# Performance work log

Hardware: AMD Instinct MI355X
Metric: run time of the kernel (lower is better)

Reference implementation:

```python
import jax, jax.numpy as jnp
import numpy as np

B, C, L, D = 8, 256, 2048, 128  # batch, in_channels, seq_len, n_factor


def setup_inputs() -> dict:
    key = jax.random.key(0)
    ks = jax.random.split(key, 8)
    s = 1.0 / np.sqrt(C)
    return {
        "x_inner": jax.random.normal(ks[0], (B, C, L), jnp.float32),
        "x_outer": jax.random.normal(ks[1], (B, C, L), jnp.float32),
        "Wq": jax.random.normal(ks[2], (D, C), jnp.float32) * s,
        "bq": jax.random.normal(ks[3], (D,), jnp.float32) * 0.01,
        "Wk": jax.random.normal(ks[4], (D, C), jnp.float32) * s,
        "bk": jax.random.normal(ks[5], (D,), jnp.float32) * 0.01,
        "Wv": jax.random.normal(ks[6], (D, C), jnp.float32) * s,
        "bv": jax.random.normal(ks[7], (D,), jnp.float32) * 0.01,
    }


def reference(x_inner, x_outer, Wq, bq, Wk, bk, Wv, bv):
    # kernel-size-1 Conv1d == per-position linear over channels; permute -> [B, L, D]
    q = jnp.einsum('bcl,dc->bld', x_inner, Wq) + bq  # [B, Lq, D]
    k = jnp.einsum('bcl,dc->bld', x_outer, Wk) + bk  # [B, Lk, D]
    v = jnp.einsum('bcl,dc->bld', x_outer, Wv) + bv  # [B, Lk, D]
    scores = jnp.einsum('bqd,bkd->bqk', q, k) / jnp.sqrt(jnp.asarray(D, q.dtype))
    attn = jax.nn.softmax(scores, axis=2)            # [B, Lq, Lk]
    return jnp.einsum('bqk,bkd->bqd', attn, v)       # [B, Lq, D]
```

## Files before the change

### kernel.cpp

```cpp
#include <hip/hip_runtime.h>
#include <hip/hip_bf16.h>

#define NB 8
#define NC 256
#define NL 2048
#define ND 128
#define NROWS (NB * NL)
#define QKV_ELEMS ((size_t)NB * NL * ND)
#define W_ELEMS (ND * NC)
#define XS_STRIDE 264

typedef __attribute__((ext_vector_type(8))) short bf16x8;
typedef __attribute__((ext_vector_type(4))) float f32x4;

__device__ __forceinline__ unsigned short f2bf(float f) {
    union { float f; unsigned u; } v; v.f = f;
    unsigned r = v.u + 0x7fffu + ((v.u >> 16) & 1u);
    return (unsigned short)(r >> 16);
}

__device__ __forceinline__ void load_lds16(const unsigned short* g, unsigned short* l) {
    __builtin_amdgcn_global_load_lds((const __attribute__((address_space(1))) unsigned int*)g,
                                     (__attribute__((address_space(3))) unsigned int*)l, 16, 0, 0);
}

__global__ void cast_w3(const float* __restrict__ wq, const float* __restrict__ wk,
                        const float* __restrict__ wv, unsigned short* __restrict__ dst) {
    int i = blockIdx.x * blockDim.x + threadIdx.x;
    if (i >= 3 * W_ELEMS) return;
    int sel = i / W_ELEMS, off = i - sel * W_ELEMS;
    const float* s = (sel == 0) ? wq : (sel == 1) ? wk : wv;
    dst[i] = f2bf(s[off]);
}

__global__ __launch_bounds__(256, 4) void proj_direct(const float* __restrict__ xi,
                                                      const float* __restrict__ xo,
                                                      const unsigned short* __restrict__ Wall,
                                                      const float* __restrict__ bq,
                                                      const float* __restrict__ bk,
                                                      const float* __restrict__ bv,
                                                      unsigned short* __restrict__ Qb,
                                                      unsigned short* __restrict__ Kb,
                                                      unsigned short* __restrict__ Vtb) {
    __shared__ unsigned short xs[64 * XS_STRIDE];
    int b = blockIdx.x >> 5, lt = blockIdx.x & 31, l0 = lt * 64;
    int y = blockIdx.y;
    int wave = threadIdx.x >> 6, lane = threadIdx.x & 63;
    int ln = lane & 15, quad = lane >> 4;

    const float* xsrc = (y == 0 ? xi : xo) + (size_t)b * NC * NL + l0;
    int l4 = (lane & 15) * 4;
    int cr0 = wave * 4 + (lane >> 4);
    #pragma unroll
    for (int g = 0; g < 4; g++) {
        float4 r[4];
        #pragma unroll
        for (int gi = 0; gi < 4; gi++) {
            int c = cr0 + (g * 4 + gi) * 16;
            r[gi] = *reinterpret_cast<const float4*>(xsrc + (size_t)c * NL + l4);
        }
        #pragma unroll
        for (int gi = 0; gi < 4; gi++) {
            int c = cr0 + (g * 4 + gi) * 16;
            xs[(l4 + 0) * XS_STRIDE + c] = f2bf(r[gi].x);
            xs[(l4 + 1) * XS_STRIDE + c] = f2bf(r[gi].y);
            xs[(l4 + 2) * XS_STRIDE + c] = f2bf(r[gi].z);
            xs[(l4 + 3) * XS_STRIDE + c] = f2bf(r[gi].w);
        }
    }
    __syncthreads();

    {
        const unsigned short* Wb = Wall + (size_t)y * W_ELEMS;
        const float* bias = y ? bk : bq;
        unsigned short* out = y ? Kb : Qb;
        int m0w = wave * 16;
        f32x4 acc[8] = {};
        #pragma unroll
        for (int s = 0; s < 8; s++) {
            bf16x8 af = *reinterpret_cast<const bf16x8*>(xs + (m0w + ln) * XS_STRIDE + s * 32 + quad * 8);
            #pragma unroll
            for (int t = 0; t < 8; t++) {
                bf16x8 bfr = *reinterpret_cast<const bf16x8*>(Wb + (size_t)(t * 16 + ln) * NC + s * 32 + quad * 8);
                acc[t] = __builtin_amdgcn_mfma_f32_16x16x32_bf16(af, bfr, acc[t], 0, 0, 0);
            }
        }
        #pragma unroll
        for (int t = 0; t < 8; t++) {
            int col = t * 16 + ln;
            float bi = bias[col];
            #pragma unroll
            for (int r = 0; r < 4; r++)
                out[(size_t)(b * NL + l0 + m0w + quad * 4 + r) * ND + col] = f2bf(acc[t][r] + bi);
        }
    }
    if (y == 1) {
        const unsigned short* Wb = Wall + 2 * (size_t)W_ELEMS;
        f32x4 acc[2][4] = {};
        #pragma unroll
        for (int s = 0; s < 8; s++) {
            bf16x8 wf0 = *reinterpret_cast<const bf16x8*>(Wb + (size_t)(wave * 32 + ln) * NC + s * 32 + quad * 8);
            bf16x8 wf1 = *reinterpret_cast<const bf16x8*>(Wb + (size_t)(wave * 32 + 16 + ln) * NC + s * 32 + quad * 8);
            #pragma unroll
            for (int t = 0; t < 4; t++) {
                bf16x8 xb = *reinterpret_cast<const bf16x8*>(xs + (t * 16 + ln) * XS_STRIDE + s * 32 + quad * 8);
                acc[0][t] = __builtin_amdgcn_mfma_f32_16x16x32_bf16(wf0, xb, acc[0][t], 0, 0, 0);
                acc[1][t] = __builtin_amdgcn_mfma_f32_16x16x32_bf16(wf1, xb, acc[1][t], 0, 0, 0);
            }
        }
        #pragma unroll
        for (int u = 0; u < 2; u++)
            #pragma unroll
            for (int t = 0; t < 4; t++)
                #pragma unroll
                for (int r = 0; r < 4; r++) {
                    int d = wave * 32 + u * 16 + quad * 4 + r;
                    Vtb[(size_t)(b * ND + d) * NL + l0 + t * 16 + ln] = f2bf(acc[u][t][r] + bv[d]);
                }
    }
}

__global__ __launch_bounds__(256, 4) void flash_attn_split(const unsigned short* __restrict__ Q,
                                                           const unsigned short* __restrict__ K,
                                                           const unsigned short* __restrict__ Vt,
                                                           float* __restrict__ Opart,
                                                           float* __restrict__ mbuf,
                                                           float* __restrict__ lbuf,
                                                           int kvlen, int S) {
    __shared__ unsigned short kbuf[64 * 128];
    __shared__ unsigned short vbuf[128 * 64];
    __shared__ unsigned short pbuf[4][16 * 64];
    int bid = blockIdx.x;
    int x = bid & 7;
    int rest = bid >> 3;
    int qt = rest & 31;
    int gh = rest >> 5;
    int g = gh * 8 + x;
    int b = g / S, sp = g % S;
    int kv0 = sp * kvlen;
    int wave = threadIdx.x >> 6, lane = threadIdx.x & 63;
    int ln = lane & 15, quad = lane >> 4;
    int m0 = qt * 64 + wave * 16;
    const float scale = 0.08838834764831845f * 1.4426950408889634f;

    bf16x8 qf[4];
    const unsigned short* qrow = Q + (size_t)(b * NL + m0 + ln) * ND + quad * 8;
    #pragma unroll
    for (int s = 0; s < 4; s++) qf[s] = *reinterpret_cast<const bf16x8*>(qrow + s * 32);

    float lsum = 0.f;
    f32x4 o_acc[8] = {};

    unsigned short* pw = pbuf[wave];
    const unsigned short* kg = K + (size_t)b * NL * ND;
    const unsigned short* vg = Vt + (size_t)b * ND * NL;

    int krt = wave * 16 + (lane >> 4);
    int kjs_lane = lane & 15;
    int vdt = wave * 32 + (lane >> 3);
    int vjs_lane = lane & 7;

    for (int kt = kv0; kt < kv0 + kvlen; kt += 64) {
        #pragma unroll
        for (int i = 0; i < 4; i++) {
            int rt = krt + i * 4;
            int js = kjs_lane ^ (rt & 15);
            load_lds16(kg + (size_t)(kt + rt) * ND + js * 8, kbuf + (wave * 16 + i * 4) * 128);
        }
        #pragma unroll
        for (int i = 0; i < 4; i++) {
            int dt = vdt + i * 8;
            int js = vjs_lane ^ (dt & 7);
            load_lds16(vg + (size_t)dt * NL + kt + js * 8, vbuf + (wave * 32 + i * 8) * 64);
        }
        __syncthreads();

        f32x4 sacc[4] = {};
        #pragma unroll
        for (int t = 0; t < 4; t++) {
            int rr = t * 16 + ln;
            #pragma unroll
            for (int s = 0; s < 4; s++) {
                bf16x8 kf = *reinterpret_cast<const bf16x8*>(kbuf + rr * 128 + ((s * 4 + quad) ^ ln) * 8);
                sacc[t] = __builtin_amdgcn_mfma_f32_16x16x32_bf16(kf, qf[s], sacc[t], 0, 0, 0);
            }
        }
        #pragma unroll
        for (int t = 0; t < 4; t++) {
            #pragma unroll
            for (int r = 0; r < 4; r++) {
                float pv = __builtin_exp2f(sacc[t][r] * scale);
                lsum += pv;
                int kpos = t * 16 + quad * 4 + r;
                pw[ln * 64 + (((kpos >> 3) ^ (ln & 7)) << 3) + (kpos & 7)] = f2bf(pv);
            }
        }
        bf16x8 pb[2];
        #pragma unroll
        for (int s2 = 0; s2 < 2; s2++)
            pb[s2] = *reinterpret_cast<const bf16x8*>(pw + ln * 64 + (((s2 * 4 + quad) ^ (ln & 7)) << 3));
        #pragma unroll
        for (int t2 = 0; t2 < 8; t2++) {
            int d = t2 * 16 + ln;
            #pragma unroll
            for (int s2 = 0; s2 < 2; s2++) {
                bf16x8 vf = *reinterpret_cast<const bf16x8*>(vbuf + d * 64 + ((s2 * 4 + quad) ^ (ln & 7)) * 8);
                o_acc[t2] = __builtin_amdgcn_mfma_f32_16x16x32_bf16(vf, pb[s2], o_acc[t2], 0, 0, 0);
            }
        }
        __syncthreads();
    }
    lsum += __shfl_xor(lsum, 16);
    lsum += __shfl_xor(lsum, 32);

    float* op = Opart + (size_t)sp * QKV_ELEMS;
    int row = b * NL + m0 + ln;
    if (quad == 0) {
        mbuf[(size_t)sp * NROWS + row] = 0.f;
        lbuf[(size_t)sp * NROWS + row] = lsum;
    }
    #pragma unroll
    for (int t2 = 0; t2 < 8; t2++)
        *reinterpret_cast<f32x4*>(op + (size_t)row * ND + t2 * 16 + quad * 4) = o_acc[t2];
}

__global__ __launch_bounds__(256) void attn_merge(const float* __restrict__ Opart,
                                                  const float* __restrict__ mbuf,
                                                  const float* __restrict__ lbuf,
                                                  float* __restrict__ out, int S) {
    int idx = blockIdx.x * 256 + threadIdx.x;
    int row = idx >> 5;
    int dg = (idx & 31) * 4;
    float M = -3.0e38f;
    for (int s = 0; s < S; s++) M = fmaxf(M, mbuf[(size_t)s * NROWS + row]);
    float L = 0.f;
    float4 acc = make_float4(0.f, 0.f, 0.f, 0.f);
    for (int s = 0; s < S; s++) {
        float w = __builtin_exp2f(mbuf[(size_t)s * NROWS + row] - M);
        L += lbuf[(size_t)s * NROWS + row] * w;
        float4 o = *reinterpret_cast<const float4*>(Opart + (size_t)s * QKV_ELEMS + (size_t)row * ND + dg);
        acc.x += o.x * w; acc.y += o.y * w; acc.z += o.z * w; acc.w += o.w * w;
    }
    float inv = 1.0f / L;
    float4 res = make_float4(acc.x * inv, acc.y * inv, acc.z * inv, acc.w * inv);
    *reinterpret_cast<float4*>(out + (size_t)row * ND + dg) = res;
}

extern "C" void kernel_launch(void* const* d_in, const int* in_sizes, int n_in,
                              void* d_out, int out_size, void* d_ws, size_t ws_size,
                              hipStream_t stream) {
    const float* x_inner = (const float*)d_in[0];
    const float* x_outer = (const float*)d_in[1];
    const float* Wq = (const float*)d_in[2];
    const float* bq = (const float*)d_in[3];
    const float* Wk = (const float*)d_in[4];
    const float* bk = (const float*)d_in[5];
    const float* Wv = (const float*)d_in[6];
    const float* bv = (const float*)d_in[7];
    float* out = (float*)d_out;

    size_t need4 = 34078720u + 3 * QKV_ELEMS * 2 + 3 * W_ELEMS * 2;
    int S = (ws_size >= need4) ? 4 : 2;
    size_t union_bytes = (S == 4) ? 34078720u : 17039360u;

    char* w = (char*)d_ws;
    float* Opart = (float*)w;
    float* mbuf = (float*)(w + (size_t)S * QKV_ELEMS * 4);
    float* lbuf = mbuf + (size_t)S * NROWS;
    unsigned short* Qb = (unsigned short*)(w + union_bytes);
    unsigned short* Kb = Qb + QKV_ELEMS;
    unsigned short* Vtb = Kb + QKV_ELEMS;
    unsigned short* Wall = Vtb + QKV_ELEMS;

    cast_w3<<<(3 * W_ELEMS + 255) / 256, 256, 0, stream>>>(Wq, Wk, Wv, Wall);
    dim3 pgrid(NB * (NL / 64), 2);
    proj_direct<<<pgrid, 256, 0, stream>>>(x_inner, x_outer, Wall, bq, bk, bv, Qb, Kb, Vtb);
    flash_attn_split<<<32 * NB * S, 256, 0, stream>>>(Qb, Kb, Vtb, Opart, mbuf, lbuf, NL / S, S);
    attn_merge<<<(NROWS * ND / 4 + 255) / 256, 256, 0, stream>>>(Opart, mbuf, lbuf, out, S);
}
```

Measured before the change: 149.7 us.

## Switch attention to 32x32x16 MFMA with 128-row query tiles

The attention kernel now uses 32x32x16 bf16 MFMA tiles: each wave handles 32 query rows and each block 128 rows, and the grid becomes 2D over (batch×tile, split). The V tile is loaded through registers into a padded, swizzled LDS layout instead of direct global-to-LDS loads. The always-zero running max buffer is dropped, so the merge kernel sums partials without rescaling. Larger MFMA tiles are meant to raise matrix throughput and reuse each K/V LDS tile across more queries, at the cost of more registers, lower occupancy (launch bounds 2) and half as many blocks.

```diff
diff --git a/kernel.cpp b/kernel.cpp
--- a/kernel.cpp
+++ b/kernel.cpp
@@ -12,6 +12,7 @@
 
 typedef __attribute__((ext_vector_type(8))) short bf16x8;
 typedef __attribute__((ext_vector_type(4))) float f32x4;
+typedef __attribute__((ext_vector_type(16))) float f32x16;
 
 __device__ __forceinline__ unsigned short f2bf(float f) {
     union { float f; unsigned u; } v; v.f = f;
@@ -120,36 +121,30 @@
     }
 }
 
-__global__ __launch_bounds__(256, 4) void flash_attn_split(const unsigned short* __restrict__ Q,
+__global__ __launch_bounds__(256, 2) void flash_attn_split(const unsigned short* __restrict__ Q,
                                                            const unsigned short* __restrict__ K,
                                                            const unsigned short* __restrict__ Vt,
                                                            float* __restrict__ Opart,
-                                                           float* __restrict__ mbuf,
                                                            float* __restrict__ lbuf,
-                                                           int kvlen, int S) {
+                                                           int kvlen) {
     __shared__ unsigned short kbuf[64 * 128];
-    __shared__ unsigned short vbuf[128 * 64];
-    __shared__ unsigned short pbuf[4][16 * 64];
-    int bid = blockIdx.x;
-    int x = bid & 7;
-    int rest = bid >> 3;
-    int qt = rest & 31;
-    int gh = rest >> 5;
-    int g = gh * 8 + x;
-    int b = g / S, sp = g % S;
+    __shared__ unsigned short vbuf[128 * 72];
+    __shared__ unsigned short pbuf[4][32 * 72];
+    int b = blockIdx.x >> 4, qt = blockIdx.x & 15;
+    int sp = blockIdx.y;
     int kv0 = sp * kvlen;
     int wave = threadIdx.x >> 6, lane = threadIdx.x & 63;
-    int ln = lane & 15, quad = lane >> 4;
-    int m0 = qt * 64 + wave * 16;
+    int l31 = lane & 31, h = lane >> 5;
+    int m0 = qt * 128 + wave * 32;
     const float scale = 0.08838834764831845f * 1.4426950408889634f;
 
-    bf16x8 qf[4];
-    const unsigned short* qrow = Q + (size_t)(b * NL + m0 + ln) * ND + quad * 8;
+    bf16x8 qf[8];
+    const unsigned short* qrow = Q + (size_t)(b * NL + m0 + l31) * ND + h * 8;
     #pragma unroll
-    for (int s = 0; s < 4; s++) qf[s] = *reinterpret_cast<const bf16x8*>(qrow + s * 32);
+    for (int s = 0; s < 8; s++) qf[s] = *reinterpret_cast<const bf16x8*>(qrow + s * 16);
 
     float lsum = 0.f;
-    f32x4 o_acc[8] = {};
+    f32x16 o_acc[4] = {};
 
     unsigned short* pw = pbuf[wave];
     const unsigned short* kg = K + (size_t)b * NL * ND;
@@ -157,8 +152,8 @@
 
     int krt = wave * 16 + (lane >> 4);
     int kjs_lane = lane & 15;
-    int vdt = wave * 32 + (lane >> 3);
-    int vjs_lane = lane & 7;
+    int vd = wave * 32 + (lane >> 3);
+    int vc = lane & 7;
 
     for (int kt = kv0; kt < kv0 + kvlen; kt += 64) {
         #pragma unroll
@@ -167,79 +162,87 @@
             int js = kjs_lane ^ (rt & 15);
             load_lds16(kg + (size_t)(kt + rt) * ND + js * 8, kbuf + (wave * 16 + i * 4) * 128);
         }
-        #pragma unroll
-        for (int i = 0; i < 4; i++) {
-            int dt = vdt + i * 8;
-            int js = vjs_lane ^ (dt & 7);
-            load_lds16(vg + (size_t)dt * NL + kt + js * 8, vbuf + (wave * 32 + i * 8) * 64);
+        {
+            bf16x8 vld[4];
+            #pragma unroll
+            for (int i = 0; i < 4; i++)
+                vld[i] = *reinterpret_cast<const bf16x8*>(vg + (size_t)(vd + i * 8) * NL + kt + vc * 8);
+            #pragma unroll
+            for (int i = 0; i < 4; i++) {
+                int d = vd + i * 8;
+                int slot = vc ^ (d & 7);
+                *reinterpret_cast<bf16x8*>(vbuf + d * 72 + slot * 8) = vld[i];
+            }
         }
         __syncthreads();
 
-        f32x4 sacc[4] = {};
-        #pragma unroll
-        for (int t = 0; t < 4; t++) {
-            int rr = t * 16 + ln;
-            #pragma unroll
-            for (int s = 0; s < 4; s++) {
-                bf16x8 kf = *reinterpret_cast<const bf16x8*>(kbuf + rr * 128 + ((s * 4 + quad) ^ ln) * 8);
-                sacc[t] = __builtin_amdgcn_mfma_f32_16x16x32_bf16(kf, qf[s], sacc[t], 0, 0, 0);
-            }
-        }
-        #pragma unroll
-        for (int t = 0; t < 4; t++) {
-            #pragma unroll
-            for (int r = 0; r < 4; r++) {
-                float pv = __builtin_exp2f(sacc[t][r] * scale);
-                lsum += pv;
-                int kpos = t * 16 + quad * 4 + r;
-                pw[ln * 64 + (((kpos >> 3) ^ (ln & 7)) << 3) + (kpos & 7)] = f2bf(pv);
-            }
-        }
-        bf16x8 pb[2];
-        #pragma unroll
-        for (int s2 = 0; s2 < 2; s2++)
-            pb[s2] = *reinterpret_cast<const bf16x8*>(pw + ln * 64 + (((s2 * 4 + quad) ^ (ln & 7)) << 3));
-        #pragma unroll
-        for (int t2 = 0; t2 < 8; t2++) {
-            int d = t2 * 16 + ln;
-            #pragma unroll
-            for (int s2 = 0; s2 < 2; s2++) {
-                bf16x8 vf = *reinterpret_cast<const bf16x8*>(vbuf + d * 64 + ((s2 * 4 + quad) ^ (ln & 7)) * 8);
-                o_acc[t2] = __builtin_amdgcn_mfma_f32_16x16x32_bf16(vf, pb[s2], o_acc[t2], 0, 0, 0);
+        f32x16 sacc[2] = {};
+        #pragma unroll
+        for (int tt = 0; tt < 2; tt++) {
+            const unsigned short* krow_p = kbuf + (tt * 32 + l31) * 128;
+            #pragma unroll
+            for (int s = 0; s < 8; s++) {
+                bf16x8 kf = *reinterpret_cast<const bf16x8*>(krow_p + (((s * 2 + h) ^ (lane & 15)) << 3));
+                sacc[tt] = __builtin_amdgcn_mfma_f32_32x32x16_bf16(kf, qf[s], sacc[tt], 0, 0, 0);
+            }
+        }
+        #pragma unroll
+        for (int tt = 0; tt < 2; tt++) {
+            #pragma unroll
+            for (int g = 0; g < 4; g++) {
+                #pragma unroll
+                for (int rr = 0; rr < 4; rr++) {
+                    float pv = __builtin_exp2f(sacc[tt][g * 4 + rr] * scale);
+                    lsum += pv;
+                    int klo = h * 4 + rr;
+                    int chunk = tt * 4 + g;
+                    pw[l31 * 72 + ((chunk ^ (l31 & 7)) << 3) + klo] = f2bf(pv);
+                }
+            }
+        }
+        bf16x8 pb[4];
+        #pragma unroll
+        for (int step = 0; step < 4; step++)
+            pb[step] = *reinterpret_cast<const bf16x8*>(pw + l31 * 72 + (((step * 2 + h) ^ (l31 & 7)) << 3));
+        #pragma unroll
+        for (int dt = 0; dt < 4; dt++) {
+            const unsigned short* vrow = vbuf + (dt * 32 + l31) * 72;
+            #pragma unroll
+            for (int step = 0; step < 4; step++) {
+                bf16x8 vf = *reinterpret_cast<const bf16x8*>(vrow + (((step * 2 + h) ^ (lane & 7)) << 3));
+                o_acc[dt] = __builtin_amdgcn_mfma_f32_32x32x16_bf16(vf, pb[step], o_acc[dt], 0, 0, 0);
             }
         }
         __syncthreads();
     }
-    lsum += __shfl_xor(lsum, 16);
     lsum += __shfl_xor(lsum, 32);
 
     float* op = Opart + (size_t)sp * QKV_ELEMS;
-    int row = b * NL + m0 + ln;
-    if (quad == 0) {
-        mbuf[(size_t)sp * NROWS + row] = 0.f;
-        lbuf[(size_t)sp * NROWS + row] = lsum;
-    }
+    int qrow_g = b * NL + m0 + l31;
+    if (lane < 32) lbuf[(size_t)sp * NROWS + qrow_g] = lsum;
     #pragma unroll
-    for (int t2 = 0; t2 < 8; t2++)
-        *reinterpret_cast<f32x4*>(op + (size_t)row * ND + t2 * 16 + quad * 4) = o_acc[t2];
+    for (int dt = 0; dt < 4; dt++) {
+        #pragma unroll
+        for (int g = 0; g < 4; g++) {
+            f32x4 v4 = { o_acc[dt][g * 4 + 0], o_acc[dt][g * 4 + 1],
+                         o_acc[dt][g * 4 + 2], o_acc[dt][g * 4 + 3] };
+            *reinterpret_cast<f32x4*>(op + (size_t)qrow_g * ND + dt * 32 + g * 8 + h * 4) = v4;
+        }
+    }
 }
 
 __global__ __launch_bounds__(256) void attn_merge(const float* __restrict__ Opart,
-                                                  const float* __restrict__ mbuf,
                                                   const float* __restrict__ lbuf,
                                                   float* __restrict__ out, int S) {
     int idx = blockIdx.x * 256 + threadIdx.x;
     int row = idx >> 5;
     int dg = (idx & 31) * 4;
-    float M = -3.0e38f;
-    for (int s = 0; s < S; s++) M = fmaxf(M, mbuf[(size_t)s * NROWS + row]);
     float L = 0.f;
     float4 acc = make_float4(0.f, 0.f, 0.f, 0.f);
     for (int s = 0; s < S; s++) {
-        float w = __builtin_exp2f(mbuf[(size_t)s * NROWS + row] - M);
-        L += lbuf[(size_t)s * NROWS + row] * w;
+        L += lbuf[(size_t)s * NROWS + row];
         float4 o = *reinterpret_cast<const float4*>(Opart + (size_t)s * QKV_ELEMS + (size_t)row * ND + dg);
-        acc.x += o.x * w; acc.y += o.y * w; acc.z += o.z * w; acc.w += o.w * w;
+        acc.x += o.x; acc.y += o.y; acc.z += o.z; acc.w += o.w;
     }
     float inv = 1.0f / L;
     float4 res = make_float4(acc.x * inv, acc.y * inv, acc.z * inv, acc.w * inv);
@@ -265,8 +268,7 @@
 
     char* w = (char*)d_ws;
     float* Opart = (float*)w;
-    float* mbuf = (float*)(w + (size_t)S * QKV_ELEMS * 4);
-    float* lbuf = mbuf + (size_t)S * NROWS;
+    float* lbuf = (float*)(w + (size_t)S * QKV_ELEMS * 4);
     unsigned short* Qb = (unsigned short*)(w + union_bytes);
     unsigned short* Kb = Qb + QKV_ELEMS;
     unsigned short* Vtb = Kb + QKV_ELEMS;
@@ -275,6 +277,7 @@
     cast_w3<<<(3 * W_ELEMS + 255) / 256, 256, 0, stream>>>(Wq, Wk, Wv, Wall);
     dim3 pgrid(NB * (NL / 64), 2);
     proj_direct<<<pgrid, 256, 0, stream>>>(x_inner, x_outer, Wall, bq, bk, bv, Qb, Kb, Vtb);
-    flash_attn_split<<<32 * NB * S, 256, 0, stream>>>(Qb, Kb, Vtb, Opart, mbuf, lbuf, NL / S, S);
-    attn_merge<<<(NROWS * ND / 4 + 255) / 256, 256, 0, stream>>>(Opart, mbuf, lbuf, out, S);
-}
+    dim3 fgrid(NB * (NL / 128), S);
+    flash_attn_split<<<fgrid, 256, 0, stream>>>(Qb, Kb, Vtb, Opart, lbuf, NL / S);
+    attn_merge<<<(NROWS * ND / 4 + 255) / 256, 256, 0, stream>>>(Opart, lbuf, out, S);
+}
```

Result: slower. 157.3 us (+5.1%).
